# Kernel tuning notes

Hardware: AMD Instinct MI355X
Metric: run time of the kernel (lower is better)

## Reference

```python
import jax, jax.numpy as jnp
import numpy as np

N_NODES = 100000
N_EDGES = 3200000
D = 64
NUM_RELS = 20
HID_ATTR = 32
OUT_ATTR = 10


def setup_inputs() -> dict:
    key = jax.random.key(0)
    ks = jax.random.split(key, 10)
    h = jax.random.normal(ks[0], (N_NODES, D), dtype=jnp.float32)
    src = jax.random.randint(ks[1], (N_EDGES,), 0, N_NODES)
    dst = jax.random.randint(ks[2], (N_EDGES,), 0, N_NODES)
    etype = jax.random.randint(ks[3], (N_EDGES,), 0, NUM_RELS)
    # RGCN relation weights (num_bases == num_rels, so no basis decomposition)
    s1 = (2.0 / (D + D)) ** 0.5 * (2.0 ** 0.5)  # xavier w/ relu gain, approx
    W1 = jax.random.normal(ks[4], (NUM_RELS, D, D), dtype=jnp.float32) * s1
    W2 = jax.random.normal(ks[5], (NUM_RELS, D, D), dtype=jnp.float32) * s1
    # Attributor MLP params (torch Linear: y = x @ W.T + b; stored here as [in,out])
    A1_w = jax.random.normal(ks[6], (D, HID_ATTR), dtype=jnp.float32) * (1.0 / D ** 0.5)
    A1_b = jnp.zeros((HID_ATTR,), dtype=jnp.float32)
    A2_w = jax.random.normal(ks[7], (HID_ATTR, OUT_ATTR), dtype=jnp.float32) * (1.0 / HID_ATTR ** 0.5)
    A2_b = jnp.zeros((OUT_ATTR,), dtype=jnp.float32)
    return {"h": h, "src": src, "dst": dst, "etype": etype,
            "W1": W1, "W2": W2, "A1_w": A1_w, "A1_b": A1_b,
            "A2_w": A2_w, "A2_b": A2_b}


def _rgcn_layer(h, W, src, dst, etype, activation):
    # Transform all nodes by every relation once (avoids [E,d,d] weight gather),
    # then gather the relation-specific transformed source feature per edge.
    n = h.shape[0]
    t = jnp.einsum('nd,rdo->rno', h, W)          # [R, N, d_out]
    msg = t[etype, src]                           # [E, d_out] irregular gather
    agg = jax.ops.segment_sum(msg, dst, num_segments=n)  # scatter-sum to nodes
    return activation(agg) if activation is not None else agg


def reference(h, src, dst, etype, W1, W2, A1_w, A1_b, A2_w, A2_b):
    # hidden RGCN layer (relu), output RGCN layer (no activation, no bias)
    h1 = _rgcn_layer(h, W1, src, dst, etype, jax.nn.relu)
    h2 = _rgcn_layer(h1, W2, src, dst, etype, None)
    # mean_nodes over the single graph -> [1, D]; Attributor MLP (dropout in eval = identity)
    g = jnp.mean(h2, axis=0, keepdims=True)
    a = jax.nn.relu(g @ A1_w + A1_b)
    a = jax.nn.sigmoid(a @ A2_w + A2_b)
    return (h2, a)
```

## Files before the change

### kernel.cpp

```cpp
#include <hip/hip_runtime.h>
#include <hip/hip_bf16.h>
#include <math.h>
#include <stdint.h>

#define N_NODES 100000
#define N_EDGES 3200000
#define D 64
#define NUM_RELS 20
#define HID_ATTR 32
#define OUT_ATTR 10
#define PADR 72
#define NFB (N_NODES / 16)

#define BUCKET_DSTS 256
#define NB 391
#define PA_THREADS 512
#define PA_EPT 16
#define PA_CHUNK (PA_THREADS * PA_EPT)
#define PA_GRID 391
#define PB_BINS (BUCKET_DSTS * NUM_RELS)

typedef __attribute__((ext_vector_type(8))) short bf16x8;
typedef __attribute__((ext_vector_type(4))) float f32x4;

static __device__ __forceinline__ unsigned short f2bf(float x) {
    unsigned u = __builtin_bit_cast(unsigned, x);
    unsigned r = (u + 0x7FFFu + ((u >> 16) & 1u)) >> 16;
    return (unsigned short)r;
}
static __device__ __forceinline__ float bf2f(unsigned short b) {
    return __builtin_bit_cast(float, (unsigned)b << 16);
}
static __device__ __forceinline__ float bf2f_lo(unsigned u) {
    return __builtin_bit_cast(float, u << 16);
}
static __device__ __forceinline__ float bf2f_hi(unsigned u) {
    return __builtin_bit_cast(float, u & 0xFFFF0000u);
}
static __device__ __forceinline__ unsigned cvt_pk_bf16(float lo, float hi) {
    unsigned r;
    asm("v_cvt_pk_bf16_f32 %0, %1, %2" : "=v"(r) : "v"(lo), "v"(hi));
    return r;
}


__global__ void hist_bucket_kernel(const int* __restrict__ dst, int* __restrict__ hist) {
    __shared__ int h[NB];
    for (int i = threadIdx.x; i < NB; i += PA_THREADS) h[i] = 0;
    __syncthreads();
    int base = blockIdx.x * PA_CHUNK;
#pragma unroll
    for (int k = 0; k < PA_EPT; ++k) {
        int e = base + k * PA_THREADS + threadIdx.x;
        if (e < N_EDGES) atomicAdd(&h[dst[e] >> 8], 1);
    }
    __syncthreads();
    for (int i = threadIdx.x; i < NB; i += PA_THREADS)
        if (h[i]) atomicAdd(&hist[i], h[i]);
}

__global__ void scan_bucket_kernel(const int* __restrict__ hist, int* __restrict__ bbase,
                                   int* __restrict__ bcur, int* __restrict__ sched_off) {
    __shared__ int s[512];
    int t = threadIdx.x;
    int v = (t < NB) ? hist[t] : 0;
    s[t] = v;
    __syncthreads();
    for (int d2 = 1; d2 < 512; d2 <<= 1) {
        int x = (t >= d2) ? s[t - d2] : 0;
        __syncthreads();
        s[t] += x;
        __syncthreads();
    }
    if (t < NB) {
        int b = s[t] - v;
        bbase[t] = b;
        bcur[t] = b;
    }
    if (t == 0) {
        bbase[NB] = N_EDGES;
        sched_off[NFB * 32] = N_EDGES;
    }
}

__global__ __launch_bounds__(PA_THREADS) void passA_kernel(
    const int* __restrict__ src, const int* __restrict__ dst,
    const int* __restrict__ etype, int* __restrict__ bcur,
    unsigned* __restrict__ tmp) {
    __shared__ int h[NB];
    __shared__ int gb[NB];
    __shared__ int c[NB];
    for (int i = threadIdx.x; i < NB; i += PA_THREADS) h[i] = 0;
    __syncthreads();
    int base = blockIdx.x * PA_CHUNK;
    int d[PA_EPT];
#pragma unroll
    for (int k = 0; k < PA_EPT; ++k) {
        int e = base + k * PA_THREADS + threadIdx.x;
        d[k] = (e < N_EDGES) ? dst[e] : -1;
        if (d[k] >= 0) atomicAdd(&h[d[k] >> 8], 1);
    }
    __syncthreads();
    for (int i = threadIdx.x; i < NB; i += PA_THREADS) {
        int n = h[i];
        gb[i] = n ? atomicAdd(&bcur[i], n) : 0;
        c[i] = 0;
    }
    __syncthreads();
#pragma unroll
    for (int k = 0; k < PA_EPT; ++k) {
        int e = base + k * PA_THREADS + threadIdx.x;
        if (d[k] >= 0) {
            int b = d[k] >> 8;
            int sv = src[e], r = etype[e];
            int pos = gb[b] + atomicAdd(&c[b], 1);
            tmp[pos] = ((unsigned)(d[k] & 255) << 22) | ((unsigned)sv << 5) | (unsigned)r;
        }
    }
}

__global__ __launch_bounds__(512) void passB_kernel(
    const unsigned* __restrict__ tmp, const int* __restrict__ bbase,
    unsigned* __restrict__ edgedata, int* __restrict__ sched_off) {
    __shared__ int binpos[PB_BINS];
    __shared__ int blen[PB_BINS];
    __shared__ unsigned sk[16 * 64];
    __shared__ int swo[16 * 64];
    __shared__ int gs[512];
    __shared__ int ssum[512];
    __shared__ int fbb[16];
    int t = threadIdx.x;
    int b = blockIdx.x;
    int beg = bbase[b], end = bbase[b + 1];
    for (int i = t; i < PB_BINS; i += 512) binpos[i] = 0;
    __syncthreads();
    for (int i = beg + t; i < end; i += 512) {
        unsigned v = tmp[i];
        int key = (int)(v >> 22) * NUM_RELS + (int)(v & 31u);
        atomicAdd(&binpos[key], 1);
    }
    __syncthreads();
    for (int i = t; i < PB_BINS; i += 512) blen[i] = binpos[i];
    __syncthreads();
    int loc[10];
    int sum = 0;
#pragma unroll
    for (int j = 0; j < 10; ++j) {
        loc[j] = sum;
        sum += binpos[t * 10 + j];
    }
    ssum[t] = sum;
    __syncthreads();
    for (int d2 = 1; d2 < 512; d2 <<= 1) {
        int x = (t >= d2) ? ssum[t - d2] : 0;
        __syncthreads();
        ssum[t] += x;
        __syncthreads();
    }
    int tbase = beg + ((t > 0) ? ssum[t - 1] : 0);
#pragma unroll
    for (int j = 0; j < 10; ++j) binpos[t * 10 + j] = tbase + loc[j];
    __syncthreads();
    if (t < 16) fbb[t] = binpos[t * 320];
    __syncthreads();
    for (int w = t; w < 1024; w += 512) {
        int fb = w >> 6, wloc = w & 63;
        int nl = wloc >> 2, qt = wloc & 3;
        int b0 = (fb * 16 + nl) * NUM_RELS + qt * 5;
        int len = blen[b0] + blen[b0 + 1] + blen[b0 + 2] + blen[b0 + 3] + blen[b0 + 4];
        sk[fb * 64 + wloc] = ((unsigned)len << 8) | (unsigned)wloc;
    }
    {
        int fb = t >> 5, k = t & 31;
        unsigned* s = &sk[fb * 64];
        for (int size = 2; size <= 64; size <<= 1) {
            for (int stride = size >> 1; stride > 0; stride >>= 1) {
                __syncthreads();
                int i1 = ((k & ~(stride - 1)) << 1) | (k & (stride - 1));
                int i2 = i1 | stride;
                unsigned x = s[i1], y = s[i2];
                bool descb = (i1 & size) == 0;
                if (descb ? (x < y) : (x > y)) { s[i1] = y; s[i2] = x; }
            }
        }
    }
    __syncthreads();
    {
        int fb = t >> 5, k = t & 31;
        unsigned kA = sk[fb * 64 + k], kB = sk[fb * 64 + 63 - k];
        int lenA = (int)(kA >> 8), widA = (int)(kA & 63u);
        int lenB = (int)(kB >> 8), widB = (int)(kB & 63u);
        int tot = lenA + lenB;
        gs[t] = tot;
        __syncthreads();
        for (int d2 = 1; d2 < 32; d2 <<= 1) {
            int x = (k >= d2) ? gs[t - d2] : 0;
            __syncthreads();
            gs[t] += x;
            __syncthreads();
        }
        int gbase = gs[t] - tot;
        swo[fb * 64 + widA] = gbase;
        swo[fb * 64 + widB] = gbase + lenA;
        int gfb = b * 16 + fb;
        if (gfb < NFB) sched_off[gfb * 32 + k] = fbb[fb] + gbase;
    }
    __syncthreads();
    for (int i = t; i < PB_BINS; i += 512) {
        int node = i / 20, rel = i - node * 20;
        int fb = node >> 4, nl = node & 15;
        int qt = rel / 5, rr = rel - qt * 5;
        int wid = nl * 4 + qt;
        int base = fbb[fb] + swo[fb * 64 + wid];
        int b0 = node * 20 + qt * 5;
        for (int r = 0; r < rr; ++r) base += blen[b0 + r];
        binpos[i] = base;
    }
    __syncthreads();
    for (int i = beg + t; i < end; i += 512) {
        unsigned v = tmp[i];
        int dl = (int)(v >> 22), rel = (int)(v & 31u);
        int ro = rel * (16 * PADR) + (dl & 15) * PADR;
        int key = dl * NUM_RELS + rel;
        int pos = atomicAdd(&binpos[key], 1);
        edgedata[pos] = ((v >> 5) & 0x1FFFFu) | ((unsigned)ro << 17);
    }
}


__global__ void f2b_kernel(const float* __restrict__ in, unsigned short* __restrict__ out,
                           int n4) {
    int i = blockIdx.x * 256 + threadIdx.x;
    if (i >= n4) return;
    float4 v = ((const float4*)in)[i];
    ushort4 o;
    o.x = f2bf(v.x); o.y = f2bf(v.y); o.z = f2bf(v.z); o.w = f2bf(v.w);
    ((ushort4*)out)[i] = o;
}

__global__ void wconv_kernel(const float* __restrict__ W, unsigned short* __restrict__ Wb) {
    int r = blockIdx.x;
    for (int i = threadIdx.x; i < D * D; i += 256) {
        int d2 = i >> 6, o = i & 63;
        Wb[(size_t)r * (D * D) + o * D + d2] = f2bf(W[(size_t)r * (D * D) + d2 * D + o]);
    }
}

__global__ __launch_bounds__(512, 6) void fused_layer(
    const unsigned short* __restrict__ xb, const unsigned short* __restrict__ Wb,
    const unsigned* __restrict__ edgedata, const int* __restrict__ sched_off,
    unsigned short* __restrict__ xbout, float* __restrict__ h2out, int mode) {
    __shared__ __align__(16) unsigned short A[NUM_RELS * 16 * PADR];
    int wave = threadIdx.x >> 6, lane = threadIdx.x & 63;
    int grp = lane >> 4, l4 = lane & 15;
    int gidx = wave * 4 + grp;
    int colb = l4 * 4;

    for (int i = threadIdx.x; i < NUM_RELS * 16 * PADR / 8; i += 512)
        ((int4*)A)[i] = (int4){0, 0, 0, 0};
    __syncthreads();

    int beg = sched_off[blockIdx.x * 32 + gidx];
    int end = sched_off[blockIdx.x * 32 + gidx + 1];
    int cnt = end - beg;
    int nb = (cnt + 7) >> 3;
    int nbmax = max(nb, __shfl_xor(nb, 16));
    nbmax = max(nbmax, __shfl_xor(nbmax, 32));
    int endm1 = end - 1;

    float a0 = 0.f, a1 = 0.f, a2 = 0.f, a3 = 0.f;
    unsigned roprev = 0xFFFFFFFFu;
    unsigned short* Ac = A + (unsigned)colb;

    auto rowload = [&](unsigned ewv) -> uint2 {
        return *(const uint2*)(xb + ((ewv & 0x1FFFFu) << 6) + (unsigned)colb);
    };
    auto proc = [&](unsigned (&ewc)[8], uint2 (&xv)[8], int valid) {
#pragma unroll
        for (int j = 0; j < 8; ++j) {
            unsigned ro = ewc[j] >> 17;
            bool real = j < valid;
            unsigned mx = real ? xv[j].x : 0u;
            unsigned my = real ? xv[j].y : 0u;
            bool keep = (ro == roprev);
            a0 = (keep ? a0 : 0.f) + bf2f_lo(mx);
            a1 = (keep ? a1 : 0.f) + bf2f_hi(mx);
            a2 = (keep ? a2 : 0.f) + bf2f_lo(my);
            a3 = (keep ? a3 : 0.f) + bf2f_hi(my);
            uint2 o;
            o.x = cvt_pk_bf16(a0, a1);
            o.y = cvt_pk_bf16(a2, a3);
            *(uint2*)(Ac + ro) = o;
            roprev = ro;
        }
    };

    unsigned ewA[8], ewB[8];
    uint2 xvA[8], xvB[8];
    if (nb > 0) {
#pragma unroll
        for (int j = 0; j < 8; ++j) ewA[j] = edgedata[min(beg + j, endm1)];
    }
    if (nb > 1) {
#pragma unroll
        for (int j = 0; j < 8; ++j) ewB[j] = edgedata[min(beg + 8 + j, endm1)];
    }
    if (nb > 0) {
#pragma unroll
        for (int j = 0; j < 8; ++j) xvA[j] = rowload(ewA[j]);
    }

    for (int g = 0; g < nbmax;) {
        {
            bool act = g < nb;
            if (act) {
                unsigned ewc[8];
#pragma unroll
                for (int j = 0; j < 8; ++j) ewc[j] = ewA[j];
                int nbase = beg + (g + 2) * 8;
                if (g + 2 < nb) {
#pragma unroll
                    for (int j = 0; j < 8; ++j)
                        ewA[j] = edgedata[min(nbase + j, endm1)];
                }
                if (g + 1 < nb) {
#pragma unroll
                    for (int j = 0; j < 8; ++j) xvB[j] = rowload(ewB[j]);
                }
                proc(ewc, xvA, cnt - g * 8);
            }
        }
        ++g;
        if (g >= nbmax) break;
        {
            bool act = g < nb;
            if (act) {
                unsigned ewc[8];
#pragma unroll
                for (int j = 0; j < 8; ++j) ewc[j] = ewB[j];
                int nbase = beg + (g + 2) * 8;
                if (g + 2 < nb) {
#pragma unroll
                    for (int j = 0; j < 8; ++j)
                        ewB[j] = edgedata[min(nbase + j, endm1)];
                }
                if (g + 1 < nb) {
#pragma unroll
                    for (int j = 0; j < 8; ++j) xvA[j] = rowload(ewA[j]);
                }
                proc(ewc, xvB, cnt - g * 8);
            }
        }
        ++g;
    }
    __syncthreads();

    if (wave < 4) {
        int lrow = lane & 15, lhi = lane >> 4;
        f32x4 C = {0.f, 0.f, 0.f, 0.f};
        for (int q = 0; q < NUM_RELS; ++q) {
            const unsigned short* Arow = &A[(q * 16 + lrow) * PADR + lhi * 8];
            bf16x8 aa0 = *(const bf16x8*)(Arow);
            bf16x8 aa1 = *(const bf16x8*)(Arow + 32);
            const unsigned short* wrow = Wb + ((size_t)q << 12)
                                         + (size_t)(wave * 16 + lrow) * D + lhi * 8;
            bf16x8 b0 = *(const bf16x8*)(wrow);
            bf16x8 b1 = *(const bf16x8*)(wrow + 32);
            C = __builtin_amdgcn_mfma_f32_16x16x32_bf16(aa0, b0, C, 0, 0, 0);
            C = __builtin_amdgcn_mfma_f32_16x16x32_bf16(aa1, b1, C, 0, 0, 0);
        }
#pragma unroll
        for (int reg = 0; reg < 4; ++reg) {
            int onode = blockIdx.x * 16 + lhi * 4 + reg;
            int col = wave * 16 + lrow;
            if (mode == 1)
                xbout[(size_t)onode * D + col] = f2bf(fmaxf(C[reg], 0.f));
            else
                h2out[(size_t)onode * D + col] = C[reg];
        }
    }
}


__global__ void colsum_kernel(const float* __restrict__ h2,
                              float* __restrict__ g, int n) {
    __shared__ float s[256];
    int tid = threadIdx.x;
    int col = tid & 63;
    int rowgrp = (blockIdx.x * blockDim.x + tid) >> 6;
    int nrowgrp = (gridDim.x * blockDim.x) >> 6;
    float acc = 0.0f;
    for (int row = rowgrp; row < n; row += nrowgrp)
        acc += h2[(size_t)row * D + col];
    s[tid] = acc;
    __syncthreads();
    if (tid < 64) {
        acc = s[tid] + s[tid + 64] + s[tid + 128] + s[tid + 192];
        atomicAdd(&g[col], acc);
    }
}

__global__ void mlp_kernel(const float* __restrict__ g,
                           const float* __restrict__ A1w,
                           const float* __restrict__ A1b,
                           const float* __restrict__ A2w,
                           const float* __restrict__ A2b,
                           float* __restrict__ out, float invN) {
    __shared__ float a1[HID_ATTR];
    int t = threadIdx.x;
    if (t < HID_ATTR) {
        float acc = A1b[t];
#pragma unroll
        for (int d2 = 0; d2 < D; ++d2)
            acc = fmaf(g[d2] * invN, A1w[d2 * HID_ATTR + t], acc);
        a1[t] = fmaxf(acc, 0.0f);
    }
    __syncthreads();
    if (t < OUT_ATTR) {
        float acc = A2b[t];
#pragma unroll
        for (int j = 0; j < HID_ATTR; ++j)
            acc = fmaf(a1[j], A2w[j * OUT_ATTR + t], acc);
        out[t] = 1.0f / (1.0f + expf(-acc));
    }
}


extern "C" void kernel_launch(void* const* d_in, const int* in_sizes, int n_in,
                              void* d_out, int out_size, void* d_ws, size_t ws_size,
                              hipStream_t stream) {
    const float* h   = (const float*)d_in[0];
    const int* src   = (const int*)d_in[1];
    const int* dst   = (const int*)d_in[2];
    const int* etype = (const int*)d_in[3];
    const float* W1  = (const float*)d_in[4];
    const float* W2  = (const float*)d_in[5];
    const float* A1w = (const float*)d_in[6];
    const float* A1b = (const float*)d_in[7];
    const float* A2w = (const float*)d_in[8];
    const float* A2b = (const float*)d_in[9];

    float* out_h2 = (float*)d_out;
    float* out_a  = out_h2 + (size_t)N_NODES * D;

    int* base       = (int*)d_ws;
    float* gsum     = (float*)base;
    int* hist_b     = base + 64;
    int* bbase      = base + 512;
    int* bcur       = base + 960;
    int* sched_off  = base + 1408;
    unsigned* tmp   = (unsigned*)(base + 201472);
    unsigned* edgedata = (unsigned*)(base + 3401472);
    unsigned short* xb  = (unsigned short*)(base + 6601472);
    unsigned short* xb2 = (unsigned short*)(base + 9801472);
    unsigned short* w1b = (unsigned short*)(base + 13001472);
    unsigned short* w2b = (unsigned short*)(base + 13042432);

    hipMemsetAsync(hist_b, 0, NB * sizeof(int), stream);
    hipMemsetAsync(gsum, 0, 64 * sizeof(float), stream);

    hist_bucket_kernel<<<PA_GRID, PA_THREADS, 0, stream>>>(dst, hist_b);
    scan_bucket_kernel<<<1, 512, 0, stream>>>(hist_b, bbase, bcur, sched_off);
    passA_kernel<<<PA_GRID, PA_THREADS, 0, stream>>>(src, dst, etype, bcur, tmp);
    passB_kernel<<<NB, 512, 0, stream>>>(tmp, bbase, edgedata, sched_off);

    wconv_kernel<<<NUM_RELS, 256, 0, stream>>>(W1, w1b);
    wconv_kernel<<<NUM_RELS, 256, 0, stream>>>(W2, w2b);
    f2b_kernel<<<(N_NODES * D / 4 + 255) / 256, 256, 0, stream>>>(h, xb, N_NODES * D / 4);

    fused_layer<<<NFB, 512, 0, stream>>>(xb, w1b, edgedata, sched_off,
                                         xb2, nullptr, 1);
    fused_layer<<<NFB, 512, 0, stream>>>(xb2, w2b, edgedata, sched_off,
                                         nullptr, out_h2, 2);

    colsum_kernel<<<512, 256, 0, stream>>>(out_h2, gsum, N_NODES);
    mlp_kernel<<<1, 64, 0, stream>>>(gsum, A1w, A1b, A2w, A2b,
                                     out_a, 1.0f / (float)N_NODES);
}
```

Before: 576.0 us.

## Deepen edge gather pipeline with smaller 4-edge batches and triple buffering

Restructures the per-group edge aggregation loop from double-buffered batches of 8 edges to batches of 4, with a 3-stage rotation: edge indices are prefetched three batches ahead and feature rows two batches ahead. The intent is to keep more gather loads in flight relative to the accumulate step while using fewer registers per batch. The trade is more loop and branch overhead per edge and a 6-phase unrolled macro body that may increase code size.

New measurement: 577.3 us. Within noise of the previous version (+0.2%).

```diff
diff --git a/kernel.cpp b/kernel.cpp
--- a/kernel.cpp
+++ b/kernel.cpp
@@ -263,7 +263,7 @@
     int beg = sched_off[blockIdx.x * 32 + gidx];
     int end = sched_off[blockIdx.x * 32 + gidx + 1];
     int cnt = end - beg;
-    int nb = (cnt + 7) >> 3;
+    int nb = (cnt + 3) >> 2;
     int nbmax = max(nb, __shfl_xor(nb, 16));
     nbmax = max(nbmax, __shfl_xor(nbmax, 32));
     int endm1 = end - 1;
@@ -275,9 +275,9 @@
     auto rowload = [&](unsigned ewv) -> uint2 {
         return *(const uint2*)(xb + ((ewv & 0x1FFFFu) << 6) + (unsigned)colb);
     };
-    auto proc = [&](unsigned (&ewc)[8], uint2 (&xv)[8], int valid) {
-#pragma unroll
-        for (int j = 0; j < 8; ++j) {
+    auto proc = [&](const unsigned (&ewc)[4], const uint2 (&xv)[4], int valid) {
+#pragma unroll
+        for (int j = 0; j < 4; ++j) {
             unsigned ro = ewc[j] >> 17;
             bool real = j < valid;
             unsigned mx = real ? xv[j].x : 0u;
@@ -295,64 +295,60 @@
         }
     };
 
-    unsigned ewA[8], ewB[8];
-    uint2 xvA[8], xvB[8];
+    unsigned e0[4], e1[4], e2[4];
+    uint2 v0[4], v1[4];
     if (nb > 0) {
 #pragma unroll
-        for (int j = 0; j < 8; ++j) ewA[j] = edgedata[min(beg + j, endm1)];
+        for (int j = 0; j < 4; ++j) e0[j] = edgedata[min(beg + j, endm1)];
     }
     if (nb > 1) {
 #pragma unroll
-        for (int j = 0; j < 8; ++j) ewB[j] = edgedata[min(beg + 8 + j, endm1)];
+        for (int j = 0; j < 4; ++j) e1[j] = edgedata[min(beg + 4 + j, endm1)];
+    }
+    if (nb > 2) {
+#pragma unroll
+        for (int j = 0; j < 4; ++j) e2[j] = edgedata[min(beg + 8 + j, endm1)];
     }
     if (nb > 0) {
 #pragma unroll
-        for (int j = 0; j < 8; ++j) xvA[j] = rowload(ewA[j]);
-    }
-
-    for (int g = 0; g < nbmax;) {
-        {
-            bool act = g < nb;
-            if (act) {
-                unsigned ewc[8];
-#pragma unroll
-                for (int j = 0; j < 8; ++j) ewc[j] = ewA[j];
-                int nbase = beg + (g + 2) * 8;
-                if (g + 2 < nb) {
-#pragma unroll
-                    for (int j = 0; j < 8; ++j)
-                        ewA[j] = edgedata[min(nbase + j, endm1)];
-                }
-                if (g + 1 < nb) {
-#pragma unroll
-                    for (int j = 0; j < 8; ++j) xvB[j] = rowload(ewB[j]);
-                }
-                proc(ewc, xvA, cnt - g * 8);
-            }
-        }
-        ++g;
-        if (g >= nbmax) break;
-        {
-            bool act = g < nb;
-            if (act) {
-                unsigned ewc[8];
-#pragma unroll
-                for (int j = 0; j < 8; ++j) ewc[j] = ewB[j];
-                int nbase = beg + (g + 2) * 8;
-                if (g + 2 < nb) {
-#pragma unroll
-                    for (int j = 0; j < 8; ++j)
-                        ewB[j] = edgedata[min(nbase + j, endm1)];
-                }
-                if (g + 1 < nb) {
-#pragma unroll
-                    for (int j = 0; j < 8; ++j) xvA[j] = rowload(ewA[j]);
-                }
-                proc(ewc, xvB, cnt - g * 8);
-            }
-        }
-        ++g;
-    }
+        for (int j = 0; j < 4; ++j) v0[j] = rowload(e0[j]);
+    }
+    if (nb > 1) {
+#pragma unroll
+        for (int j = 0; j < 4; ++j) v1[j] = rowload(e1[j]);
+    }
+
+#define PHASE(GG, EW0, EW2, XV0)                                              \
+    {                                                                         \
+        int gg = (GG);                                                        \
+        if (gg < nbmax) {                                                     \
+            unsigned ewc[4];                                                  \
+            uint2 xvc[4];                                                     \
+            _Pragma("unroll") for (int j = 0; j < 4; ++j) {                   \
+                ewc[j] = EW0[j]; xvc[j] = XV0[j];                             \
+            }                                                                 \
+            if (gg + 3 < nb) {                                                \
+                int lb = beg + (gg + 3) * 4;                                  \
+                _Pragma("unroll") for (int j = 0; j < 4; ++j)                 \
+                    EW0[j] = edgedata[min(lb + j, endm1)];                    \
+            }                                                                 \
+            if (gg + 2 < nb) {                                                \
+                _Pragma("unroll") for (int j = 0; j < 4; ++j)                 \
+                    XV0[j] = rowload(EW2[j]);                                 \
+            }                                                                 \
+            if (gg < nb) proc(ewc, xvc, cnt - gg * 4);                        \
+        }                                                                     \
+    }
+
+    for (int g = 0; g < nbmax; g += 6) {
+        PHASE(g + 0, e0, e2, v0)
+        PHASE(g + 1, e1, e0, v1)
+        PHASE(g + 2, e2, e1, v0)
+        PHASE(g + 3, e0, e2, v1)
+        PHASE(g + 4, e1, e0, v0)
+        PHASE(g + 5, e2, e1, v1)
+    }
+#undef PHASE
     __syncthreads();
 
     if (wave < 4) {
```

## Stage per-block edge metadata in LDS and drop register double-buffering

Applied to the files above, without the earlier changes.

Each block now cooperatively copies its contiguous edge-metadata range (up to 2048 words) into shared memory before the gather loop, then reads per-edge words from LDS instead of global memory. If the block has more edges than fit, it falls back to reading global memory. The explicit two-stage register prefetch pipeline (ewA/ewB, xvA/xvB) is replaced by a simple loop that loads 8 edge words, issues 8 row gathers, then accumulates. This cuts register pressure and redundant global loads, but gives up the overlap of gather latency with computation and adds 8KB of LDS per block, which may reduce occupancy.

Result: slower. 599.0 us (+4.0%).

```diff
diff --git a/kernel.cpp b/kernel.cpp
--- a/kernel.cpp
+++ b/kernel.cpp
@@ -11,6 +11,7 @@
 #define OUT_ATTR 10
 #define PADR 72
 #define NFB (N_NODES / 16)
+#define WCAP 2048
 
 #define BUCKET_DSTS 256
 #define NB 391
@@ -251,107 +252,70 @@
     const unsigned* __restrict__ edgedata, const int* __restrict__ sched_off,
     unsigned short* __restrict__ xbout, float* __restrict__ h2out, int mode) {
     __shared__ __align__(16) unsigned short A[NUM_RELS * 16 * PADR];
+    __shared__ unsigned wlds[WCAP];
     int wave = threadIdx.x >> 6, lane = threadIdx.x & 63;
     int grp = lane >> 4, l4 = lane & 15;
     int gidx = wave * 4 + grp;
     int colb = l4 * 4;
 
+    int blk_beg = sched_off[blockIdx.x * 32];
+    int blk_end = sched_off[blockIdx.x * 32 + 32];
+    int beg = sched_off[blockIdx.x * 32 + gidx];
+    int end = sched_off[blockIdx.x * 32 + gidx + 1];
+
     for (int i = threadIdx.x; i < NUM_RELS * 16 * PADR / 8; i += 512)
         ((int4*)A)[i] = (int4){0, 0, 0, 0};
-    __syncthreads();
-
-    int beg = sched_off[blockIdx.x * 32 + gidx];
-    int end = sched_off[blockIdx.x * 32 + gidx + 1];
+    int cnt_blk = blk_end - blk_beg;
+    int nstage = min(cnt_blk, WCAP);
+    for (int i = threadIdx.x; i < nstage; i += 512)
+        wlds[i] = edgedata[blk_beg + i];
+    __syncthreads();
+
+    const unsigned* wptr = (cnt_blk <= WCAP) ? (const unsigned*)wlds
+                                             : (edgedata + blk_beg);
+    int lbase = beg - blk_beg;
     int cnt = end - beg;
     int nb = (cnt + 7) >> 3;
     int nbmax = max(nb, __shfl_xor(nb, 16));
     nbmax = max(nbmax, __shfl_xor(nbmax, 32));
-    int endm1 = end - 1;
+    int cm1 = cnt - 1;
 
     float a0 = 0.f, a1 = 0.f, a2 = 0.f, a3 = 0.f;
     unsigned roprev = 0xFFFFFFFFu;
     unsigned short* Ac = A + (unsigned)colb;
 
-    auto rowload = [&](unsigned ewv) -> uint2 {
-        return *(const uint2*)(xb + ((ewv & 0x1FFFFu) << 6) + (unsigned)colb);
-    };
-    auto proc = [&](unsigned (&ewc)[8], uint2 (&xv)[8], int valid) {
-#pragma unroll
-        for (int j = 0; j < 8; ++j) {
-            unsigned ro = ewc[j] >> 17;
-            bool real = j < valid;
-            unsigned mx = real ? xv[j].x : 0u;
-            unsigned my = real ? xv[j].y : 0u;
-            bool keep = (ro == roprev);
-            a0 = (keep ? a0 : 0.f) + bf2f_lo(mx);
-            a1 = (keep ? a1 : 0.f) + bf2f_hi(mx);
-            a2 = (keep ? a2 : 0.f) + bf2f_lo(my);
-            a3 = (keep ? a3 : 0.f) + bf2f_hi(my);
-            uint2 o;
-            o.x = cvt_pk_bf16(a0, a1);
-            o.y = cvt_pk_bf16(a2, a3);
-            *(uint2*)(Ac + ro) = o;
-            roprev = ro;
-        }
-    };
-
-    unsigned ewA[8], ewB[8];
-    uint2 xvA[8], xvB[8];
-    if (nb > 0) {
-#pragma unroll
-        for (int j = 0; j < 8; ++j) ewA[j] = edgedata[min(beg + j, endm1)];
-    }
-    if (nb > 1) {
-#pragma unroll
-        for (int j = 0; j < 8; ++j) ewB[j] = edgedata[min(beg + 8 + j, endm1)];
-    }
-    if (nb > 0) {
-#pragma unroll
-        for (int j = 0; j < 8; ++j) xvA[j] = rowload(ewA[j]);
-    }
-
-    for (int g = 0; g < nbmax;) {
-        {
-            bool act = g < nb;
-            if (act) {
-                unsigned ewc[8];
-#pragma unroll
-                for (int j = 0; j < 8; ++j) ewc[j] = ewA[j];
-                int nbase = beg + (g + 2) * 8;
-                if (g + 2 < nb) {
-#pragma unroll
-                    for (int j = 0; j < 8; ++j)
-                        ewA[j] = edgedata[min(nbase + j, endm1)];
-                }
-                if (g + 1 < nb) {
-#pragma unroll
-                    for (int j = 0; j < 8; ++j) xvB[j] = rowload(ewB[j]);
-                }
-                proc(ewc, xvA, cnt - g * 8);
+    for (int g = 0; g < nbmax; ++g) {
+        if (g < nb) {
+            unsigned w[8];
+            uint2 xv[8];
+#pragma unroll
+            for (int j = 0; j < 8; ++j) {
+                int k = min(g * 8 + j, cm1);
+                w[j] = wptr[lbase + k];
             }
-        }
-        ++g;
-        if (g >= nbmax) break;
-        {
-            bool act = g < nb;
-            if (act) {
-                unsigned ewc[8];
-#pragma unroll
-                for (int j = 0; j < 8; ++j) ewc[j] = ewB[j];
-                int nbase = beg + (g + 2) * 8;
-                if (g + 2 < nb) {
-#pragma unroll
-                    for (int j = 0; j < 8; ++j)
-                        ewB[j] = edgedata[min(nbase + j, endm1)];
-                }
-                if (g + 1 < nb) {
-#pragma unroll
-                    for (int j = 0; j < 8; ++j) xvA[j] = rowload(ewA[j]);
-                }
-                proc(ewc, xvB, cnt - g * 8);
+#pragma unroll
+            for (int j = 0; j < 8; ++j)
+                xv[j] = *(const uint2*)(xb + ((w[j] & 0x1FFFFu) << 6)
+                                        + (unsigned)colb);
+            int valid = cnt - g * 8;
+#pragma unroll
+            for (int j = 0; j < 8; ++j) {
+                unsigned ro = w[j] >> 17;
+                bool real = j < valid;
+                unsigned mx = real ? xv[j].x : 0u;
+                unsigned my = real ? xv[j].y : 0u;
+                bool keep = (ro == roprev);
+                a0 = (keep ? a0 : 0.f) + bf2f_lo(mx);
+                a1 = (keep ? a1 : 0.f) + bf2f_hi(mx);
+                a2 = (keep ? a2 : 0.f) + bf2f_lo(my);
+                a3 = (keep ? a3 : 0.f) + bf2f_hi(my);
+                uint2 o;
+                o.x = cvt_pk_bf16(a0, a1);
+                o.y = cvt_pk_bf16(a2, a3);
+                *(uint2*)(Ac + ro) = o;
+                roprev = ro;
             }
         }
-        ++g;
     }
     __syncthreads();
 
```
